# Kernel tuning notes

Measured on AMD Instinct MI355X. Metric: run time of the kernel, lower is better.

Reference implementation:

```python
import jax, jax.numpy as jnp
import numpy as np

N_NODES = 50000

def setup_inputs() -> dict:
    key = jax.random.key(0)
    k1, k2, k3, k4, k5, k6 = jax.random.split(key, 6)
    N, E, D_IN, D_OUT = N_NODES, 800000, 128, 128
    feature = jax.random.normal(k1, (N, D_IN), dtype=jnp.float32)
    src = jax.random.randint(k2, (E,), 0, N, dtype=jnp.int64)
    dst = jax.random.randint(k3, (E,), 0, N, dtype=jnp.int64)
    w = jax.random.uniform(k4, (E,), dtype=jnp.float32)
    W = jax.random.normal(k5, (D_OUT, D_IN), dtype=jnp.float32) * (1.0 / np.sqrt(D_IN))
    b = jax.random.normal(k6, (D_OUT,), dtype=jnp.float32) * 0.01
    return {"feature": feature, "src": src, "dst": dst, "w": w, "W": W, "b": b}

def reference(feature, src, dst, w, W, b):
    # gcn_msg: gather source node features, scale by per-edge weight  [E, D]
    msg = feature[src] * w[:, None]
    # fn.sum: scatter-sum messages into destination nodes  [N, D]
    agg = jax.ops.segment_sum(msg, dst, num_segments=N_NODES)
    # NodeApplyModule: linear + activation
    h = agg @ W.T + b
    return jax.nn.relu(h)
```

## Files before the change

kernel.cpp:

```cpp
#include <hip/hip_runtime.h>

#define D 128
#define TILE_M 64
#define BS_STRIDE 129
#define AS_STRIDE 68
#define WS_STRIDE 136
#define DS_STRIDE 136
#define GEMM_BLOCKS 768
#define CAP 64

typedef __attribute__((ext_vector_type(8))) short short8;
typedef __attribute__((ext_vector_type(4))) float floatx4;
typedef __attribute__((ext_vector_type(4))) unsigned short ushortx4;

__device__ __forceinline__ unsigned short f2bf(float f) {
    unsigned u = __float_as_uint(f);
    u += 0x7fffu + ((u >> 16) & 1u);
    return (unsigned short)(u >> 16);
}

__global__ __launch_bounds__(256) void gemm_bucket(
    const float* __restrict__ feat, const float* __restrict__ Wm,
    unsigned short* __restrict__ tf,
    const int* __restrict__ src, const int* __restrict__ dst,
    const float* __restrict__ w, int* __restrict__ cnt,
    unsigned* __restrict__ ep, int N, int E)
{
    __shared__ unsigned short Ws[128 * WS_STRIDE];
    __shared__ unsigned short Ds[64 * DS_STRIDE];

    {
        const int xcd = blockIdx.x & 7;
        const int blk = blockIdx.x >> 3;
        const int nblk = GEMM_BLOCKS >> 3;
        const int lo = (int)((long long)xcd * N / 8);
        const int hi = (int)((long long)(xcd + 1) * N / 8);
        const int E4 = E & ~3;
        for (int e4 = (blk * 256 + threadIdx.x) * 4; e4 < E4; e4 += nblk * 256 * 4) {
            const int4   d4 = *reinterpret_cast<const int4*>(dst + e4);
            const int4   s4 = *reinterpret_cast<const int4*>(src + e4);
            const float4 w4 = *reinterpret_cast<const float4*>(w + e4);
#pragma unroll
            for (int j = 0; j < 4; ++j) {
                int   d  = (j == 0) ? d4.x : (j == 1) ? d4.y : (j == 2) ? d4.z : d4.w;
                if (d >= lo && d < hi) {
                    int   sj = (j == 0) ? s4.x : (j == 1) ? s4.y : (j == 2) ? s4.z : s4.w;
                    float wj = (j == 0) ? w4.x : (j == 1) ? w4.y : (j == 2) ? w4.z : w4.w;
                    unsigned rec = ((unsigned)f2bf(wj) << 16) | (unsigned)sj;
                    int pos = atomicAdd(&cnt[d], 1);
                    if (pos < CAP)
                        ep[(size_t)pos * (size_t)N + (size_t)d] = rec;
                }
            }
        }
        if (threadIdx.x == 0 && blk == 0) {
            for (int e = E4; e < E; ++e) {
                int d = dst[e];
                if (d >= lo && d < hi) {
                    unsigned rec = ((unsigned)f2bf(w[e]) << 16) | (unsigned)src[e];
                    int pos = atomicAdd(&cnt[d], 1);
                    if (pos < CAP)
                        ep[(size_t)pos * (size_t)N + (size_t)d] = rec;
                }
            }
        }
    }

    const int tid = threadIdx.x;
    for (int idx = tid; idx < 128 * 128 / 4; idx += 256) {
        int r = idx >> 5;
        int c = (idx & 31) * 4;
        const float4 v = reinterpret_cast<const float4*>(Wm)[idx];
        ushortx4 s;
        s[0] = f2bf(v.x); s[1] = f2bf(v.y); s[2] = f2bf(v.z); s[3] = f2bf(v.w);
        *reinterpret_cast<ushortx4*>(&Ws[r * WS_STRIDE + c]) = s;
    }
    __syncthreads();

    const int lane = tid & 63;
    const int wave = tid >> 6;
    const int kq = (lane >> 4) * 8;
    const int ntiles = (N + 63) >> 6;

    for (int t = blockIdx.x; t < ntiles; t += GEMM_BLOCKS) {
        const int node0 = t * 64;
        const int mr = node0 + wave * 16 + (lane & 15);
        const float* arow = feat + (size_t)(mr < N ? mr : (N - 1)) * D + kq;

        short8 a[4];
#pragma unroll
        for (int kt = 0; kt < 4; ++kt) {
            const float* p = arow + kt * 32;
            const float4 lo = *reinterpret_cast<const float4*>(p);
            const float4 hi = *reinterpret_cast<const float4*>(p + 4);
            short8 v;
            v[0] = (short)f2bf(lo.x); v[1] = (short)f2bf(lo.y);
            v[2] = (short)f2bf(lo.z); v[3] = (short)f2bf(lo.w);
            v[4] = (short)f2bf(hi.x); v[5] = (short)f2bf(hi.y);
            v[6] = (short)f2bf(hi.z); v[7] = (short)f2bf(hi.w);
            a[kt] = v;
        }

        floatx4 acc[8];
#pragma unroll
        for (int nt = 0; nt < 8; ++nt) {
            acc[nt][0] = 0.f; acc[nt][1] = 0.f; acc[nt][2] = 0.f; acc[nt][3] = 0.f;
        }
#pragma unroll
        for (int nt = 0; nt < 8; ++nt) {
            const unsigned short* brow = &Ws[(nt * 16 + (lane & 15)) * WS_STRIDE + kq];
#pragma unroll
            for (int kt = 0; kt < 4; ++kt) {
                short8 b = *reinterpret_cast<const short8*>(brow + kt * 32);
                acc[nt] = __builtin_amdgcn_mfma_f32_16x16x32_bf16(a[kt], b, acc[nt], 0, 0, 0);
            }
        }

        __syncthreads();
        const int mlocal = wave * 16 + (lane >> 4) * 4;
        const int col = lane & 15;
#pragma unroll
        for (int r = 0; r < 4; ++r) {
            unsigned short* drow = &Ds[(mlocal + r) * DS_STRIDE + col];
#pragma unroll
            for (int nt = 0; nt < 8; ++nt)
                drow[nt * 16] = f2bf(acc[nt][r]);
        }
        __syncthreads();

        for (int idx = tid; idx < 64 * 16; idx += 256) {
            int row = idx >> 4;
            int chunk = idx & 15;
            int m = node0 + row;
            if (m < N) {
                uint4 v = *reinterpret_cast<const uint4*>(&Ds[row * DS_STRIDE + chunk * 8]);
                *reinterpret_cast<uint4*>(tf + (size_t)m * D + chunk * 8) = v;
            }
        }
    }
}

__global__ __launch_bounds__(256) void csr_gather_bf16(
    const unsigned short* __restrict__ tf, const unsigned* __restrict__ ep,
    const int* __restrict__ cnt, const float* __restrict__ bias,
    float* __restrict__ out, int N)
{
    int node = blockIdx.x * 16 + (threadIdx.x >> 4);
    if (node >= N) return;
    const int lane = threadIdx.x & 15;
    const int c = lane << 3;
    const unsigned* col = ep + node;
    int end = cnt[node];
    end = end < CAP ? end : CAP;
    int p = 0;
    float a0 = 0.f, a1 = 0.f, a2 = 0.f, a3 = 0.f;
    float a4 = 0.f, a5 = 0.f, a6 = 0.f, a7 = 0.f;

#define ACC8(Q, W)                                       \
    a0 += __uint_as_float((Q).x << 16) * (W);            \
    a1 += __uint_as_float((Q).x & 0xffff0000u) * (W);    \
    a2 += __uint_as_float((Q).y << 16) * (W);            \
    a3 += __uint_as_float((Q).y & 0xffff0000u) * (W);    \
    a4 += __uint_as_float((Q).z << 16) * (W);            \
    a5 += __uint_as_float((Q).z & 0xffff0000u) * (W);    \
    a6 += __uint_as_float((Q).w << 16) * (W);            \
    a7 += __uint_as_float((Q).w & 0xffff0000u) * (W);

    for (; p + 7 < end; p += 8) {
        unsigned r[8];
#pragma unroll
        for (int j = 0; j < 8; ++j) r[j] = col[(size_t)(p + j) * N];
        uint4 q[8];
        float wv[8];
#pragma unroll
        for (int j = 0; j < 8; ++j) {
            q[j] = *reinterpret_cast<const uint4*>(tf + (size_t)(r[j] & 0xffffu) * D + c);
            wv[j] = __uint_as_float(r[j] & 0xffff0000u);
        }
#pragma unroll
        for (int j = 0; j < 8; ++j) { ACC8(q[j], wv[j]) }
    }
    for (; p + 3 < end; p += 4) {
        unsigned r[4];
#pragma unroll
        for (int j = 0; j < 4; ++j) r[j] = col[(size_t)(p + j) * N];
        uint4 q[4];
        float wv[4];
#pragma unroll
        for (int j = 0; j < 4; ++j) {
            q[j] = *reinterpret_cast<const uint4*>(tf + (size_t)(r[j] & 0xffffu) * D + c);
            wv[j] = __uint_as_float(r[j] & 0xffff0000u);
        }
#pragma unroll
        for (int j = 0; j < 4; ++j) { ACC8(q[j], wv[j]) }
    }
    for (; p < end; ++p) {
        unsigned r = col[(size_t)p * N];
        float wv = __uint_as_float(r & 0xffff0000u);
        uint4 q = *reinterpret_cast<const uint4*>(tf + (size_t)(r & 0xffffu) * D + c);
        ACC8(q, wv)
    }
#undef ACC8

    const float4 bv0 = *reinterpret_cast<const float4*>(bias + c);
    const float4 bv1 = *reinterpret_cast<const float4*>(bias + c + 4);
    float4 r0, r1;
    r0.x = fmaxf(a0 + bv0.x, 0.f);
    r0.y = fmaxf(a1 + bv0.y, 0.f);
    r0.z = fmaxf(a2 + bv0.z, 0.f);
    r0.w = fmaxf(a3 + bv0.w, 0.f);
    r1.x = fmaxf(a4 + bv1.x, 0.f);
    r1.y = fmaxf(a5 + bv1.y, 0.f);
    r1.z = fmaxf(a6 + bv1.z, 0.f);
    r1.w = fmaxf(a7 + bv1.w, 0.f);
    float* o = out + (size_t)node * D + c;
    *reinterpret_cast<float4*>(o) = r0;
    *reinterpret_cast<float4*>(o + 4) = r1;
}

__global__ __launch_bounds__(256) void edge_scatter(
    const float* __restrict__ feat, const int* __restrict__ src,
    const int* __restrict__ dst, const float* __restrict__ w,
    float* __restrict__ agg, int E)
{
    long long idx = (long long)blockIdx.x * 256 + threadIdx.x;
    int e = (int)(idx >> 5);
    if (e >= E) return;
    int c = ((int)idx & 31) << 2;
    int s = src[e];
    int d = dst[e];
    float wv = w[e];
    const float4 f = *reinterpret_cast<const float4*>(feat + (size_t)s * D + c);
    float* a = agg + (size_t)d * D + c;
    atomicAdd(a + 0, f.x * wv);
    atomicAdd(a + 1, f.y * wv);
    atomicAdd(a + 2, f.z * wv);
    atomicAdd(a + 3, f.w * wv);
}

__global__ __launch_bounds__(256) void node_linear(
    const float* __restrict__ in, const float* __restrict__ Wm,
    const float* __restrict__ bias, float* __restrict__ out, int N)
{
    __shared__ float Bs[64 * BS_STRIDE];
    __shared__ float As[TILE_M * AS_STRIDE];
    const int tid = threadIdx.x;
    const int tx = tid & 15;
    const int ty = tid >> 4;
    const int node0 = blockIdx.x * TILE_M;
    float acc[4][8];
#pragma unroll
    for (int i = 0; i < 4; ++i)
#pragma unroll
        for (int jj = 0; jj < 8; ++jj) acc[i][jj] = 0.0f;
    for (int kh = 0; kh < 2; ++kh) {
        const int kbase = kh * 64;
        for (int i = tid; i < 128 * 64; i += 256) {
            int j = i >> 6, k = i & 63;
            Bs[k * BS_STRIDE + j] = Wm[j * 128 + kbase + k];
        }
        for (int i = tid; i < TILE_M * 64; i += 256) {
            int m = i >> 6, k = i & 63;
            int n = node0 + m;
            As[m * AS_STRIDE + k] = (n < N) ? in[(size_t)n * D + kbase + k] : 0.0f;
        }
        __syncthreads();
        for (int k0 = 0; k0 < 64; k0 += 4) {
            float a[4][4];
#pragma unroll
            for (int i = 0; i < 4; ++i) {
                const float4 v = *reinterpret_cast<const float4*>(&As[(ty * 4 + i) * AS_STRIDE + k0]);
                a[i][0] = v.x; a[i][1] = v.y; a[i][2] = v.z; a[i][3] = v.w;
            }
#pragma unroll
            for (int kk = 0; kk < 4; ++kk) {
                float bv[8];
#pragma unroll
                for (int jj = 0; jj < 8; ++jj) bv[jj] = Bs[(k0 + kk) * BS_STRIDE + tx + 16 * jj];
#pragma unroll
                for (int i = 0; i < 4; ++i)
#pragma unroll
                    for (int jj = 0; jj < 8; ++jj) acc[i][jj] += a[i][kk] * bv[jj];
            }
        }
        __syncthreads();
    }
    float bv[8];
#pragma unroll
    for (int jj = 0; jj < 8; ++jj) bv[jj] = bias[tx + 16 * jj];
#pragma unroll
    for (int i = 0; i < 4; ++i) {
        int n = node0 + ty * 4 + i;
        if (n < N) {
            float* o = out + (size_t)n * D;
#pragma unroll
            for (int jj = 0; jj < 8; ++jj) {
                float v = acc[i][jj] + bv[jj];
                o[tx + 16 * jj] = v > 0.0f ? v : 0.0f;
            }
        }
    }
}

extern "C" void kernel_launch(void* const* d_in, const int* in_sizes, int n_in,
                              void* d_out, int out_size, void* d_ws, size_t ws_size,
                              hipStream_t stream) {
    const float* feat = (const float*)d_in[0];
    const int*   src  = (const int*)d_in[1];
    const int*   dst  = (const int*)d_in[2];
    const float* w    = (const float*)d_in[3];
    const float* Wm   = (const float*)d_in[4];
    const float* bias = (const float*)d_in[5];
    float* out = (float*)d_out;

    const int N = in_sizes[0] / D;
    const int E = in_sizes[1];

    const size_t ep_b  = (size_t)N * CAP * 4;
    const size_t cnt_b = (size_t)N * sizeof(int);
    const size_t tf_b  = (size_t)N * D * 2;
    auto align_up = [](size_t x) { return (x + 255) & ~(size_t)255; };

    const size_t need_full = align_up(ep_b) + align_up(cnt_b) + align_up(tf_b);

    if (ws_size >= need_full && N <= 65536 &&
        (long long)E <= (long long)N * (CAP / 4)) {
        char* p = (char*)d_ws;
        unsigned* ep  = (unsigned*)p;  p += align_up(ep_b);
        int*      cnt = (int*)p;       p += align_up(cnt_b);
        unsigned short* tf = (unsigned short*)p;

        (void)hipMemsetAsync(cnt, 0, cnt_b, stream);
        gemm_bucket<<<GEMM_BLOCKS, 256, 0, stream>>>(
            feat, Wm, tf, src, dst, w, cnt, ep, N, E);
        csr_gather_bf16<<<(N + 15) / 16, 256, 0, stream>>>(tf, ep, cnt, bias, out, N);
    } else {
        (void)hipMemsetAsync(out, 0, (size_t)N * D * sizeof(float), stream);
        long long st = (long long)E * 32;
        edge_scatter<<<(int)((st + 255) / 256), 256, 0, stream>>>(feat, src, dst, w, out, E);
        node_linear<<<(N + TILE_M - 1) / TILE_M, 256, 0, stream>>>(out, Wm, bias, out, N);
    }
}
```

Baseline: 161.3 us.

## Split edge bucketing out of the GEMM kernel into a separate launch

The edge-bucketing phase, which was fused into the GEMM kernel with each XCD filtering its own range of destination nodes, moves into its own one-thread-per-edge kernel that runs before a pure GEMM kernel. This drops the eightfold re-read of src, dst and w that the per-XCD filtering caused, and gives the atomics the full grid. In exchange it adds a launch and loses the overlap between bucketing and the GEMM, along with the XCD locality of the cnt atomics.

```diff
diff --git a/kernel.cpp b/kernel.cpp
--- a/kernel.cpp
+++ b/kernel.cpp
@@ -19,52 +19,26 @@
     return (unsigned short)(u >> 16);
 }
 
-__global__ __launch_bounds__(256) void gemm_bucket(
-    const float* __restrict__ feat, const float* __restrict__ Wm,
-    unsigned short* __restrict__ tf,
+__global__ __launch_bounds__(256) void bucket_build(
     const int* __restrict__ src, const int* __restrict__ dst,
     const float* __restrict__ w, int* __restrict__ cnt,
     unsigned* __restrict__ ep, int N, int E)
 {
+    int e = blockIdx.x * 256 + threadIdx.x;
+    if (e >= E) return;
+    int d = dst[e];
+    unsigned rec = ((unsigned)f2bf(w[e]) << 16) | (unsigned)src[e];
+    int pos = atomicAdd(&cnt[d], 1);
+    if (pos < CAP)
+        ep[(size_t)pos * (size_t)N + (size_t)d] = rec;
+}
+
+__global__ __launch_bounds__(256) void gemm_tf(
+    const float* __restrict__ feat, const float* __restrict__ Wm,
+    unsigned short* __restrict__ tf, int N)
+{
     __shared__ unsigned short Ws[128 * WS_STRIDE];
     __shared__ unsigned short Ds[64 * DS_STRIDE];
-
-    {
-        const int xcd = blockIdx.x & 7;
-        const int blk = blockIdx.x >> 3;
-        const int nblk = GEMM_BLOCKS >> 3;
-        const int lo = (int)((long long)xcd * N / 8);
-        const int hi = (int)((long long)(xcd + 1) * N / 8);
-        const int E4 = E & ~3;
-        for (int e4 = (blk * 256 + threadIdx.x) * 4; e4 < E4; e4 += nblk * 256 * 4) {
-            const int4   d4 = *reinterpret_cast<const int4*>(dst + e4);
-            const int4   s4 = *reinterpret_cast<const int4*>(src + e4);
-            const float4 w4 = *reinterpret_cast<const float4*>(w + e4);
-#pragma unroll
-            for (int j = 0; j < 4; ++j) {
-                int   d  = (j == 0) ? d4.x : (j == 1) ? d4.y : (j == 2) ? d4.z : d4.w;
-                if (d >= lo && d < hi) {
-                    int   sj = (j == 0) ? s4.x : (j == 1) ? s4.y : (j == 2) ? s4.z : s4.w;
-                    float wj = (j == 0) ? w4.x : (j == 1) ? w4.y : (j == 2) ? w4.z : w4.w;
-                    unsigned rec = ((unsigned)f2bf(wj) << 16) | (unsigned)sj;
-                    int pos = atomicAdd(&cnt[d], 1);
-                    if (pos < CAP)
-                        ep[(size_t)pos * (size_t)N + (size_t)d] = rec;
-                }
-            }
-        }
-        if (threadIdx.x == 0 && blk == 0) {
-            for (int e = E4; e < E; ++e) {
-                int d = dst[e];
-                if (d >= lo && d < hi) {
-                    unsigned rec = ((unsigned)f2bf(w[e]) << 16) | (unsigned)src[e];
-                    int pos = atomicAdd(&cnt[d], 1);
-                    if (pos < CAP)
-                        ep[(size_t)pos * (size_t)N + (size_t)d] = rec;
-                }
-            }
-        }
-    }
 
     const int tid = threadIdx.x;
     for (int idx = tid; idx < 128 * 128 / 4; idx += 256) {
@@ -331,8 +305,8 @@
         unsigned short* tf = (unsigned short*)p;
 
         (void)hipMemsetAsync(cnt, 0, cnt_b, stream);
-        gemm_bucket<<<GEMM_BLOCKS, 256, 0, stream>>>(
-            feat, Wm, tf, src, dst, w, cnt, ep, N, E);
+        bucket_build<<<(E + 255) / 256, 256, 0, stream>>>(src, dst, w, cnt, ep, N, E);
+        gemm_tf<<<GEMM_BLOCKS, 256, 0, stream>>>(feat, Wm, tf, N);
         csr_gather_bf16<<<(N + 15) / 16, 256, 0, stream>>>(tf, ep, cnt, bias, out, N);
     } else {
         (void)hipMemsetAsync(out, 0, (size_t)N * D * sizeof(float), stream);
```

New measurement: 168.1 us. +4.2%, slower.
